# Optimization experiments

Measured on AMD Instinct MI355X. Metric: run time of the kernel, lower is better.

The kernel has to match this reference:

```python
import jax, jax.numpy as jnp
import numpy as np

T_STEPS = 4
TAU = 2.0
EPS = 1e-5
NUM_HEADS = 8
SCALE = 0.125  # hardcoded self.scale in the torch module
SG_ALPHA = 4.0  # spikingjelly default sigmoid surrogate alpha


@jax.custom_vjp
def heaviside(x):
    return (x >= 0.0).astype(x.dtype)

def _hv_fwd(x):
    return heaviside(x), x

def _hv_bwd(x, g):
    s = jax.nn.sigmoid(SG_ALPHA * x)
    return (g * SG_ALPHA * s * (1.0 - s),)

heaviside.defvjp(_hv_fwd, _hv_bwd)


def lif(x_seq, v_th):
    # MultiStepLIFNode: v += (x - v)/tau; spike = H(v - v_th); hard reset to 0 (detached).
    def step(v, x):
        v = v + (x - v) / TAU
        s = heaviside(v - v_th)
        v = v * (1.0 - jax.lax.stop_gradient(s))
        return v, s
    _, out = jax.lax.scan(step, jnp.zeros_like(x_seq[0]), x_seq)
    return out


def bn(x, g, b):
    # BatchNorm1d training-mode stats over (batch, length) per channel; x: (TB, C, N)
    m = jnp.mean(x, axis=(0, 2), keepdims=True)
    var = jnp.mean((x - m) ** 2, axis=(0, 2), keepdims=True)
    return g[None, :, None] * (x - m) * jax.lax.rsqrt(var + EPS) + b[None, :, None]


def _branch(x, w, b, g, beta):
    # linear over channel dim + BN + LIF, then split heads -> (T,B,H,N,d)
    T, B, C, N = x.shape
    y = jnp.einsum('oc,tbcn->tbon', w, x) + b[None, None, :, None]
    y = bn(y.reshape(T * B, C, N), g, beta).reshape(T, B, C, N)
    y = lif(y, 1.0)
    d = C // NUM_HEADS
    return y.transpose(0, 1, 3, 2).reshape(T, B, N, NUM_HEADS, d).transpose(0, 1, 3, 2, 4)


def setup_inputs() -> dict:
    key = jax.random.key(0)
    ks = jax.random.split(key, 6)
    B, C, N = 8, 512, 1024
    bound = float(np.sqrt(6.0 / (3 * C + C)))  # xavier_uniform for (3C, C)
    return {
        'q': jax.random.normal(ks[0], (B, C, N), jnp.float32),
        'k': jax.random.normal(ks[1], (B, C, N), jnp.float32),
        'v': jax.random.normal(ks[2], (B, C, N), jnp.float32),
        'in_proj_w': jax.random.uniform(ks[3], (3 * C, C), jnp.float32, -bound, bound),
        'in_proj_b': jnp.zeros((3 * C,), jnp.float32),
        'q_gamma': jnp.ones((C,), jnp.float32),
        'q_beta': jnp.zeros((C,), jnp.float32),
        'k_gamma': jnp.ones((C,), jnp.float32),
        'k_beta': jnp.zeros((C,), jnp.float32),
        'v_gamma': jnp.ones((C,), jnp.float32),
        'v_beta': jnp.zeros((C,), jnp.float32),
        'proj_w': jax.random.normal(ks[4], (C, C), jnp.float32) * (1.0 / np.sqrt(C)),
        'proj_b': jnp.zeros((C,), jnp.float32),
        'p_gamma': jnp.ones((C,), jnp.float32),
        'p_beta': jnp.zeros((C,), jnp.float32),
    }


def reference(q, k, v, in_proj_w, in_proj_b, q_gamma, q_beta, k_gamma, k_beta,
              v_gamma, v_beta, proj_w, proj_b, p_gamma, p_beta):
    B, C, N = q.shape
    qs = jnp.broadcast_to(q[None], (T_STEPS, B, C, N))
    ks_ = jnp.broadcast_to(k[None], (T_STEPS, B, C, N))
    vs = jnp.broadcast_to(v[None], (T_STEPS, B, C, N))

    qh = _branch(qs, in_proj_w[:C], in_proj_b[:C], q_gamma, q_beta)        # (T,B,H,N,d)
    kh = _branch(ks_, in_proj_w[C:2 * C], in_proj_b[C:2 * C], k_gamma, k_beta)
    vh = _branch(vs, in_proj_w[2 * C:], in_proj_b[2 * C:], v_gamma, v_beta)

    # linear attention: (k^T v) then q @ (k^T v)
    ktv = jnp.einsum('tbhnd,tbhne->tbhde', kh, vh)            # (T,B,H,d,d)
    att = jnp.einsum('tbhnd,tbhde->tbhne', qh, ktv) * SCALE   # (T,B,H,N,d)

    x = att.transpose(0, 1, 2, 4, 3).reshape(T_STEPS, B, C, N)
    x = lif(x, 0.5)  # attn_lif with v_threshold=0.5

    z = jnp.einsum('oc,tbcn->tbon', proj_w, x) + proj_b[None, None, :, None]  # 1x1 conv
    z = bn(z.reshape(T_STEPS * B, C, N), p_gamma, p_beta).reshape(T_STEPS, B, C, N)
    return lif(z, 1.0)
```

## Files before the change

### kernel.cpp

```cpp
#include <hip/hip_runtime.h>

#define C    512
#define NDIM 1024
#define BDIM 8
#define TDIM 4
#define HDIM 8
#define CN   (C*NDIM)
#define BCN  (BDIM*CN)

typedef unsigned short u16;
typedef unsigned int   u32;
typedef unsigned long long u64;
typedef __attribute__((ext_vector_type(8))) short bf8v;
typedef __attribute__((ext_vector_type(4))) float f4v;

__device__ __forceinline__ u16 f2bf(float f) {
    u32 u = __float_as_uint(f);
    u32 r = u + 0x7FFFu + ((u >> 16) & 1u);
    return (u16)(r >> 16);
}
__device__ __forceinline__ float bf2f(u16 h) { return __uint_as_float((u32)h << 16); }

#if defined(__has_builtin)
#if __has_builtin(__builtin_amdgcn_global_load_lds)
#define HAS_GLL 1
#endif
#endif
#ifdef HAS_GLL
#define GLD(gp, lp) __builtin_amdgcn_global_load_lds( \
    (const __attribute__((address_space(1))) u32*)(gp), \
    (__attribute__((address_space(3))) u32*)(lp), 16, 0, 0)
#else
#define GLD(gp, lp) (*(uint4*)(lp) = *(const uint4*)(const void*)(gp))
#endif

__global__ __launch_bounds__(256) void gemm_in3_k(
    const float* __restrict__ W, const float* __restrict__ bias,
    const float* __restrict__ Xq, const float* __restrict__ Xk,
    const float* __restrict__ Xv, float* __restrict__ Y3)
{
    __shared__ float As[16][68];
    __shared__ float Bs[16][136];
    const int tid = threadIdx.x;
    const int bz = blockIdx.z;
    const int br = bz >> 3, b = bz & 7;
    const int m0 = blockIdx.y * 64;
    const int n0 = blockIdx.x * 128;
    const float* Xb = (br == 0 ? Xq : (br == 1 ? Xk : Xv)) + (size_t)b * CN;
    const int rowOff = br * 512;

    const int am = tid >> 2;
    const int ak = (tid & 3) * 4;
    const int bk = tid >> 4;
    const int bn = (tid & 15) * 8;
    const int tx = tid & 15, ty = tid >> 4;

    float acc[4][8];
    #pragma unroll
    for (int i = 0; i < 4; i++)
        #pragma unroll
        for (int j = 0; j < 8; j++) acc[i][j] = 0.f;

    for (int k0 = 0; k0 < 512; k0 += 16) {
        float4 a  = *(const float4*)&W [(size_t)(rowOff + m0 + am) * 512 + k0 + ak];
        float4 b0 = *(const float4*)&Xb[(size_t)(k0 + bk) * NDIM + n0 + bn];
        float4 b1 = *(const float4*)&Xb[(size_t)(k0 + bk) * NDIM + n0 + bn + 4];
        __syncthreads();
        As[ak + 0][am] = a.x; As[ak + 1][am] = a.y;
        As[ak + 2][am] = a.z; As[ak + 3][am] = a.w;
        *(float4*)&Bs[bk][bn]     = b0;
        *(float4*)&Bs[bk][bn + 4] = b1;
        __syncthreads();
        #pragma unroll
        for (int k = 0; k < 16; k++) {
            float av[4], bv[8];
            *(float4*)av = *(const float4*)&As[k][ty * 4];
            *(float4*)&bv[0] = *(const float4*)&Bs[k][tx * 8];
            *(float4*)&bv[4] = *(const float4*)&Bs[k][tx * 8 + 4];
            #pragma unroll
            for (int i = 0; i < 4; i++)
                #pragma unroll
                for (int j = 0; j < 8; j++)
                    acc[i][j] += av[i] * bv[j];
        }
    }
    #pragma unroll
    for (int i = 0; i < 4; i++) {
        float bsv = bias[rowOff + m0 + ty * 4 + i];
        float* yr = Y3 + (size_t)bz * CN + (size_t)(m0 + ty * 4 + i) * NDIM + n0 + tx * 8;
        float4 o0 = make_float4(acc[i][0] + bsv, acc[i][1] + bsv,
                                acc[i][2] + bsv, acc[i][3] + bsv);
        float4 o1 = make_float4(acc[i][4] + bsv, acc[i][5] + bsv,
                                acc[i][6] + bsv, acc[i][7] + bsv);
        *(float4*)&yr[0] = o0;
        *(float4*)&yr[4] = o1;
    }
}

__global__ __launch_bounds__(256) void split_pw_k(
    const float* __restrict__ PW, u16* __restrict__ Ps)
{
    const int idx = blockIdx.x * 256 + threadIdx.x;
    float x = PW[idx];
    u16 h1 = f2bf(x); float r1 = x - bf2f(h1);
    u16 h2 = f2bf(r1); float r2 = r1 - bf2f(h2);
    u16 h3 = f2bf(r2);
    Ps[idx] = h1; Ps[idx + 262144] = h2; Ps[idx + 2 * 262144] = h3;
}

__global__ __launch_bounds__(256, 2) void gemm_proj_mfma(
    const u16* __restrict__ Ps, const unsigned char* __restrict__ spkT,
    float* __restrict__ Z)
{
    __shared__ __align__(16) u16 Ab[2][12288];
    __shared__ __align__(16) u16 Bb[2][4096];
    const int tid = threadIdx.x;
    const int zb = blockIdx.z, t = zb >> 3, bb = zb & 7;
    const int m0 = blockIdx.y * 128, n0 = blockIdx.x * 128;

    u32 aoff[2][3];
    int lofs[2];
    #pragma unroll
    for (int r = 0; r < 2; r++) {
        const int cid = tid + (r << 8);
        const int mm = cid & 15, kg = (cid >> 4) & 3, mt = cid >> 6;
        lofs[r] = cid * 8;
        #pragma unroll
        for (int s = 0; s < 3; s++)
            aoff[r][s] = (u32)s * 262144u + (u32)(m0 + mt * 16 + mm) * 512u + kg * 8;
    }
    auto stageA = [&](int ki2, int p2) {
        const u32 kk = (u32)ki2 << 5;
        #pragma unroll
        for (int r = 0; r < 2; r++)
            #pragma unroll
            for (int s = 0; s < 3; s++)
                GLD(Ps + aoff[r][s] + kk, &Ab[p2][s * 4096 + lofs[r]]);
    };
    const int nn = tid & 15, ntl = (tid >> 4) & 7, seg = tid >> 7;
    const u32 srcB = ((u32)bb * 1024u + (u32)(n0 + ntl * 16 + nn)) * 512u + seg * 16;
    const int ldsB0 = (ntl * 64 + seg * 32 + nn) * 8;
    auto convB = [&](uint4 braw, int p2) {
        u32 bs[4] = {braw.x, braw.y, braw.z, braw.w};
        u32 w[8];
        #pragma unroll
        for (int qq = 0; qq < 4; qq++) {
            u32 v = bs[qq] >> t;
            w[qq * 2 + 0] = ((v & 1u) ? 0x3F80u : 0u) | ((v & 0x100u) ? 0x3F800000u : 0u);
            w[qq * 2 + 1] = (((v >> 16) & 1u) ? 0x3F80u : 0u) | ((v & 0x1000000u) ? 0x3F800000u : 0u);
        }
        *(uint4*)&Bb[p2][ldsB0]       = make_uint4(w[0], w[1], w[2], w[3]);
        *(uint4*)&Bb[p2][ldsB0 + 128] = make_uint4(w[4], w[5], w[6], w[7]);
    };

    const int lane = tid & 63, wv = tid >> 6;
    const int wm = wv >> 1, wn = wv & 1;
    const int q = lane >> 4, ln = lane & 15;
    int afo[4], bfo[4];
    #pragma unroll
    for (int i = 0; i < 4; i++) {
        afo[i] = ((wm * 4 + i) * 64 + q * 16 + ln) * 8;
        bfo[i] = ((wn * 4 + i) * 64 + q * 16 + ln) * 8;
    }

    f4v acc[4][4];
    #pragma unroll
    for (int i = 0; i < 4; i++)
        #pragma unroll
        for (int j = 0; j < 4; j++) acc[i][j] = (f4v){0.f, 0.f, 0.f, 0.f};

    stageA(0, 0);
    convB(*(const uint4*)&spkT[srcB], 0);
    uint4 braw;
    for (int ki = 0; ki < 16; ki++) {
        const int p = ki & 1;
        __syncthreads();
        if (ki < 15) {
            stageA(ki + 1, p ^ 1);
            braw = *(const uint4*)&spkT[srcB + ((u32)(ki + 1) << 5)];
        }
        bf8v bf[4];
        #pragma unroll
        for (int j = 0; j < 4; j++) bf[j] = *(const bf8v*)&Bb[p][bfo[j]];
        #pragma unroll
        for (int sa = 0; sa < 3; sa++) {
            bf8v af[4];
            #pragma unroll
            for (int i = 0; i < 4; i++) af[i] = *(const bf8v*)&Ab[p][sa * 4096 + afo[i]];
            #pragma unroll
            for (int i = 0; i < 4; i++)
                #pragma unroll
                for (int j = 0; j < 4; j++)
                    acc[i][j] = __builtin_amdgcn_mfma_f32_16x16x32_bf16(af[i], bf[j], acc[i][j], 0, 0, 0);
        }
        if (ki < 15) convB(braw, p ^ 1);
    }
    float* Zb = Z + (size_t)zb * CN;
    #pragma unroll
    for (int i = 0; i < 4; i++) {
        const int row = m0 + (wm * 4 + i) * 16 + q * 4;
        #pragma unroll
        for (int g = 0; g < 4; g++) {
            float* zr = Zb + (size_t)(row + g) * 1024 + n0 + ln;
            #pragma unroll
            for (int j = 0; j < 4; j++)
                zr[(wn * 4 + j) * 16] = acc[i][j][g];
        }
    }
}

__global__ __launch_bounds__(256) void chan_sum3_k(
    const float* __restrict__ X3, float* __restrict__ mean3, int outer)
{
    __shared__ float red[256];
    const int gb = blockIdx.x;
    const int o = gb & (C - 1);
    const float* X = X3 + (size_t)(gb >> 9) * BCN;
    const int tid = threadIdx.x;
    const int total = outer * NDIM;
    float s = 0.f;
    for (int i = tid; i < total; i += 256) {
        int ou = i >> 10, n = i & 1023;
        s += X[(size_t)(ou * C + o) * NDIM + n];
    }
    red[tid] = s; __syncthreads();
    for (int off = 128; off > 0; off >>= 1) {
        if (tid < off) red[tid] += red[tid + off];
        __syncthreads();
    }
    if (tid == 0) mean3[gb] = red[0] / (float)total;
}

__global__ __launch_bounds__(256) void chan_var3_k(
    const float* __restrict__ X3, const float* __restrict__ mean3,
    float* __restrict__ rstd3, int outer)
{
    __shared__ float red[256];
    const int gb = blockIdx.x;
    const int o = gb & (C - 1);
    const float* X = X3 + (size_t)(gb >> 9) * BCN;
    const int tid = threadIdx.x;
    const int total = outer * NDIM;
    const float m = mean3[gb];
    float s = 0.f;
    for (int i = tid; i < total; i += 256) {
        int ou = i >> 10, n = i & 1023;
        float d = X[(size_t)(ou * C + o) * NDIM + n] - m;
        s += d * d;
    }
    red[tid] = s; __syncthreads();
    for (int off = 128; off > 0; off >>= 1) {
        if (tid < off) red[tid] += red[tid + off];
        __syncthreads();
    }
    if (tid == 0) rstd3[gb] = 1.f / sqrtf(red[0] / (float)total + 1e-5f);
}

__global__ __launch_bounds__(256) void bn_lif_pack_k(
    const float* __restrict__ Y, const float* __restrict__ mean,
    const float* __restrict__ rstd, const float* __restrict__ gamma,
    const float* __restrict__ beta, unsigned char* __restrict__ spk)
{
    const int idx = blockIdx.x * 256 + threadIdx.x;
    const int o = (idx >> 10) & (C - 1);
    float y = Y[idx];
    float x = gamma[o] * (y - mean[o]);
    x = x * rstd[o] + beta[o];
    float v = 0.f; unsigned bits = 0;
    #pragma unroll
    for (int t = 0; t < 4; t++) {
        v += (x - v) * 0.5f;
        if (v - 1.0f >= 0.f) { bits |= (1u << t); v = 0.f; }
    }
    spk[idx] = (unsigned char)bits;
}

__global__ __launch_bounds__(256) void qpack_k(
    const unsigned char* __restrict__ spk, u64* __restrict__ qm)
{
    __shared__ unsigned char tile[64][80];
    const int tid = threadIdx.x;
    const int bh = blockIdx.x; const int h = bh & 7, b = bh >> 3;
    const int n0 = blockIdx.y * 64;
    {
        int dd = tid >> 2, sg = tid & 3;
        *(uint4*)&tile[dd][sg * 16] =
            *(const uint4*)&spk[(size_t)(b * C + h * 64 + dd) * NDIM + n0 + sg * 16];
    }
    __syncthreads();
    const int lane = tid & 63, wv = tid >> 6;
    for (int i = 0; i < 16; i++) {
        int j = wv * 16 + i;
        unsigned s = tile[lane][j];
        #pragma unroll
        for (int t = 0; t < 4; t++) {
            u64 m = __ballot((s >> t) & 1);
            if (lane == t)
                qm[(size_t)((t * BDIM + b) * HDIM + h) * NDIM + n0 + j] = m;
        }
    }
}

__global__ __launch_bounds__(256) void kv_pack_k(
    const unsigned char* __restrict__ spk, u64* __restrict__ bits)
{
    const int tid = threadIdx.x;
    const int gw = blockIdx.x * 4 + (tid >> 6);
    const int lane = tid & 63;
    const int w = gw & 15, c = (gw >> 4) & (C - 1), b = gw >> 13;
    unsigned s = spk[(size_t)(b * C + c) * NDIM + w * 64 + lane];
    #pragma unroll
    for (int t = 0; t < 4; t++) {
        u64 m = __ballot((s >> t) & 1);
        if (lane == t)
            bits[(size_t)((t * BDIM + b) * C + c) * 16 + w] = m;
    }
}

__global__ __launch_bounds__(256) void ktv_k(
    const u64* __restrict__ kb, const u64* __restrict__ vb,
    u16* __restrict__ ktv)
{
    __shared__ u64 ks[64][17];
    __shared__ u64 vs[64][17];
    const int tid = threadIdx.x;
    const int g = blockIdx.x;
    const int h = g & 7, b = (g >> 3) & 7, t = g >> 6;
    const size_t base = ((size_t)(t * BDIM + b) * C + h * 64) * 16;
    {
        int r = tid >> 2, w0 = (tid & 3) * 4;
        #pragma unroll
        for (int j = 0; j < 4; j++) {
            ks[r][w0 + j] = kb[base + r * 16 + w0 + j];
            vs[r][w0 + j] = vb[base + r * 16 + w0 + j];
        }
    }
    __syncthreads();
    const int dd = tid >> 2, e0 = (tid & 3) * 16;
    u64 kr[16];
    #pragma unroll
    for (int w = 0; w < 16; w++) kr[w] = ks[dd][w];
    #pragma unroll
    for (int i = 0; i < 16; i++) {
        int e = e0 + i;
        int s = 0;
        #pragma unroll
        for (int w = 0; w < 16; w++) s += __popcll(kr[w] & vs[e][w]);
        ktv[(size_t)(g * 64 + dd) * 64 + e] = (u16)s;
    }
}

__global__ __launch_bounds__(256) void att_lif_k(
    const u16* __restrict__ ktv, const u64* __restrict__ qm,
    unsigned char* __restrict__ spkT)
{
    __shared__ u16 ks[4][64][64];
    const int tid = threadIdx.x;
    const int bh = blockIdx.x; const int h = bh & 7, b = bh >> 3;
    const int n0 = blockIdx.y * 64;
    #pragma unroll
    for (int t = 0; t < 4; t++) {
        const u32* src = (const u32*)&ktv[(size_t)((t * BDIM + b) * HDIM + h) * 4096];
        u32* dst = (u32*)&ks[t][0][0];
        #pragma unroll
        for (int j = 0; j < 8; j++) dst[tid + 256 * j] = src[tid + 256 * j];
    }
    __syncthreads();
    const int lane = tid & 63, wv = tid >> 6;
    for (int i = 0; i < 16; i++) {
        const int n = n0 + wv * 16 + i;
        float v = 0.f; unsigned bits = 0;
        #pragma unroll
        for (int t = 0; t < 4; t++) {
            u64 m = qm[(size_t)((t * BDIM + b) * HDIM + h) * NDIM + n];
            int acc = 0;
            while (m) {
                int dd = __ffsll(m) - 1;
                m &= m - 1;
                acc += ks[t][dd][lane];
            }
            float x = (float)acc * 0.125f;
            v += (x - v) * 0.5f;
            if (v - 0.5f >= 0.f) { bits |= (1u << t); v = 0.f; }
        }
        spkT[((size_t)b * 1024 + n) * 512 + h * 64 + lane] = (unsigned char)bits;
    }
}

__global__ __launch_bounds__(256) void final_bn_lif_k(
    float* __restrict__ Z, const float* __restrict__ mean,
    const float* __restrict__ rstd, const float* __restrict__ gamma,
    const float* __restrict__ beta)
{
    const int idx = blockIdx.x * 256 + threadIdx.x;
    const int o = (idx >> 10) & (C - 1);
    const float m = mean[o], rs = rstd[o], g = gamma[o], bt = beta[o];
    float v = 0.f;
    float outs[4];
    #pragma unroll
    for (int t = 0; t < 4; t++) {
        float z = Z[(size_t)t * BCN + idx];
        float x = g * (z - m);
        x = x * rs + bt;
        v += (x - v) * 0.5f;
        float s = (v - 1.0f >= 0.f) ? 1.f : 0.f;
        v *= (1.f - s);
        outs[t] = s;
    }
    #pragma unroll
    for (int t = 0; t < 4; t++) Z[(size_t)t * BCN + idx] = outs[t];
}

extern "C" void kernel_launch(void* const* d_in, const int* in_sizes, int n_in,
                              void* d_out, int out_size, void* d_ws, size_t ws_size,
                              hipStream_t stream)
{
    const float* q     = (const float*)d_in[0];
    const float* k     = (const float*)d_in[1];
    const float* v     = (const float*)d_in[2];
    const float* W     = (const float*)d_in[3];
    const float* Wb    = (const float*)d_in[4];
    const float* qg    = (const float*)d_in[5];
    const float* qb    = (const float*)d_in[6];
    const float* kg    = (const float*)d_in[7];
    const float* kbt   = (const float*)d_in[8];
    const float* vg    = (const float*)d_in[9];
    const float* vbt   = (const float*)d_in[10];
    const float* pw    = (const float*)d_in[11];
    const float* pg    = (const float*)d_in[13];
    const float* pbeta = (const float*)d_in[14];

    char* p = (char*)d_ws;
    unsigned char* spk = (unsigned char*)p; p += (size_t)BCN;
    u64* qmv = (u64*)p;                     p += (size_t)TDIM * BDIM * HDIM * NDIM * 8;
    u64* kbits = (u64*)p;                   p += (size_t)TDIM * BDIM * C * 16 * 8;
    u64* vbits = (u64*)p;                   p += (size_t)TDIM * BDIM * C * 16 * 8;
    u16* ktv = (u16*)p;                     p += (size_t)TDIM * BDIM * HDIM * 64 * 64 * 2;
    float* mean3 = (float*)p;               p += 8192;
    float* rstd3 = (float*)p;               p += 8192;

    float* Y3 = (float*)d_out;
    float* outF = (float*)d_out;
    u16* Ps = (u16*)qmv;
    unsigned char* spkT = spk;

    const float* Gs[3] = {qg, kg, vg};
    const float* Bt[3] = {qb, kbt, vbt};

    gemm_in3_k<<<dim3(8, 8, 24), 256, 0, stream>>>(W, Wb, q, k, v, Y3);
    chan_sum3_k<<<3 * C, 256, 0, stream>>>(Y3, mean3, BDIM);
    chan_var3_k<<<3 * C, 256, 0, stream>>>(Y3, mean3, rstd3, BDIM);
    for (int br = 0; br < 3; ++br) {
        bn_lif_pack_k<<<BCN / 256, 256, 0, stream>>>(Y3 + (size_t)br * BCN,
            mean3 + br * C, rstd3 + br * C, Gs[br], Bt[br], spk);
        if (br == 0)
            qpack_k<<<dim3(64, 16), 256, 0, stream>>>(spk, qmv);
        else
            kv_pack_k<<<16384, 256, 0, stream>>>(spk, br == 1 ? kbits : vbits);
    }
    ktv_k<<<256, 256, 0, stream>>>(kbits, vbits, ktv);
    att_lif_k<<<dim3(64, 16), 256, 0, stream>>>(ktv, qmv, spkT);
    split_pw_k<<<1024, 256, 0, stream>>>(pw, Ps);
    gemm_proj_mfma<<<dim3(8, 4, 32), 256, 0, stream>>>(Ps, spkT, outF);
    chan_sum3_k<<<C, 256, 0, stream>>>(outF, mean3, TDIM * BDIM);
    chan_var3_k<<<C, 256, 0, stream>>>(outF, mean3, rstd3, TDIM * BDIM);
    final_bn_lif_k<<<BCN / 256, 256, 0, stream>>>(outF, mean3, rstd3, pg, pbeta);
}
```

Measured before the change: 585.2 us.

## Enlarge input GEMM tile to 128x128 and fuse BN-LIF with K/V bit packing

The fp32 input projection GEMM moves from 64x128 to 128x128 tiles, each thread computing a 2x2 grid of 4x4 sub-blocks, which raises arithmetic intensity and halves the grid. For the K and V branches, BN+LIF now emits the ballot-packed spike bitmasks directly, which drops the intermediate byte spike buffer and the separate kv_pack kernel launch. Larger per-thread accumulators raise register pressure and may lower occupancy.

Result: faster. 553.4 us (-5.4%).

```diff
diff --git a/kernel.cpp b/kernel.cpp
--- a/kernel.cpp
+++ b/kernel.cpp
@@ -39,62 +39,75 @@
     const float* __restrict__ Xq, const float* __restrict__ Xk,
     const float* __restrict__ Xv, float* __restrict__ Y3)
 {
-    __shared__ float As[16][68];
-    __shared__ float Bs[16][136];
+    __shared__ float As[16][132];
+    __shared__ float Bs[16][132];
     const int tid = threadIdx.x;
     const int bz = blockIdx.z;
     const int br = bz >> 3, b = bz & 7;
-    const int m0 = blockIdx.y * 64;
+    const int m0 = blockIdx.y * 128;
     const int n0 = blockIdx.x * 128;
     const float* Xb = (br == 0 ? Xq : (br == 1 ? Xk : Xv)) + (size_t)b * CN;
     const int rowOff = br * 512;
 
-    const int am = tid >> 2;
-    const int ak = (tid & 3) * 4;
-    const int bk = tid >> 4;
-    const int bn = (tid & 15) * 8;
+    const int ra = tid >> 2, ka = (tid & 3) * 4;
+    const int kb = tid >> 5, nb = (tid & 31) * 4;
     const int tx = tid & 15, ty = tid >> 4;
 
-    float acc[4][8];
-    #pragma unroll
-    for (int i = 0; i < 4; i++)
-        #pragma unroll
-        for (int j = 0; j < 8; j++) acc[i][j] = 0.f;
-
-    for (int k0 = 0; k0 < 512; k0 += 16) {
-        float4 a  = *(const float4*)&W [(size_t)(rowOff + m0 + am) * 512 + k0 + ak];
-        float4 b0 = *(const float4*)&Xb[(size_t)(k0 + bk) * NDIM + n0 + bn];
-        float4 b1 = *(const float4*)&Xb[(size_t)(k0 + bk) * NDIM + n0 + bn + 4];
-        __syncthreads();
-        As[ak + 0][am] = a.x; As[ak + 1][am] = a.y;
-        As[ak + 2][am] = a.z; As[ak + 3][am] = a.w;
-        *(float4*)&Bs[bk][bn]     = b0;
-        *(float4*)&Bs[bk][bn + 4] = b1;
-        __syncthreads();
-        #pragma unroll
-        for (int k = 0; k < 16; k++) {
-            float av[4], bv[8];
-            *(float4*)av = *(const float4*)&As[k][ty * 4];
-            *(float4*)&bv[0] = *(const float4*)&Bs[k][tx * 8];
-            *(float4*)&bv[4] = *(const float4*)&Bs[k][tx * 8 + 4];
+    float acc[2][2][4][4];
+    #pragma unroll
+    for (int mq = 0; mq < 2; mq++)
+        #pragma unroll
+        for (int nq = 0; nq < 2; nq++)
             #pragma unroll
             for (int i = 0; i < 4; i++)
                 #pragma unroll
-                for (int j = 0; j < 8; j++)
-                    acc[i][j] += av[i] * bv[j];
-        }
-    }
-    #pragma unroll
-    for (int i = 0; i < 4; i++) {
-        float bsv = bias[rowOff + m0 + ty * 4 + i];
-        float* yr = Y3 + (size_t)bz * CN + (size_t)(m0 + ty * 4 + i) * NDIM + n0 + tx * 8;
-        float4 o0 = make_float4(acc[i][0] + bsv, acc[i][1] + bsv,
-                                acc[i][2] + bsv, acc[i][3] + bsv);
-        float4 o1 = make_float4(acc[i][4] + bsv, acc[i][5] + bsv,
-                                acc[i][6] + bsv, acc[i][7] + bsv);
-        *(float4*)&yr[0] = o0;
-        *(float4*)&yr[4] = o1;
-    }
+                for (int j = 0; j < 4; j++) acc[mq][nq][i][j] = 0.f;
+
+    for (int k0 = 0; k0 < 512; k0 += 16) {
+        float4 a0 = *(const float4*)&W[(size_t)(rowOff + m0 + ra) * 512 + k0 + ka];
+        float4 a1 = *(const float4*)&W[(size_t)(rowOff + m0 + 64 + ra) * 512 + k0 + ka];
+        float4 b0 = *(const float4*)&Xb[(size_t)(k0 + kb) * NDIM + n0 + nb];
+        float4 b1 = *(const float4*)&Xb[(size_t)(k0 + 8 + kb) * NDIM + n0 + nb];
+        __syncthreads();
+        As[ka + 0][ra] = a0.x; As[ka + 1][ra] = a0.y;
+        As[ka + 2][ra] = a0.z; As[ka + 3][ra] = a0.w;
+        As[ka + 0][64 + ra] = a1.x; As[ka + 1][64 + ra] = a1.y;
+        As[ka + 2][64 + ra] = a1.z; As[ka + 3][64 + ra] = a1.w;
+        *(float4*)&Bs[kb][nb]     = b0;
+        *(float4*)&Bs[kb + 8][nb] = b1;
+        __syncthreads();
+        #pragma unroll
+        for (int k = 0; k < 16; k++) {
+            float av[2][4], bv[2][4];
+            *(float4*)av[0] = *(const float4*)&As[k][ty * 4];
+            *(float4*)av[1] = *(const float4*)&As[k][64 + ty * 4];
+            *(float4*)bv[0] = *(const float4*)&Bs[k][tx * 4];
+            *(float4*)bv[1] = *(const float4*)&Bs[k][64 + tx * 4];
+            #pragma unroll
+            for (int mq = 0; mq < 2; mq++)
+                #pragma unroll
+                for (int nq = 0; nq < 2; nq++)
+                    #pragma unroll
+                    for (int i = 0; i < 4; i++)
+                        #pragma unroll
+                        for (int j = 0; j < 4; j++)
+                            acc[mq][nq][i][j] += av[mq][i] * bv[nq][j];
+        }
+    }
+    #pragma unroll
+    for (int mq = 0; mq < 2; mq++)
+        #pragma unroll
+        for (int i = 0; i < 4; i++) {
+            const int mrow = mq * 64 + ty * 4 + i;
+            float bsv = bias[rowOff + m0 + mrow];
+            float* yr = Y3 + (size_t)bz * CN + (size_t)(m0 + mrow) * NDIM + n0;
+            #pragma unroll
+            for (int nq = 0; nq < 2; nq++) {
+                float4 o4 = make_float4(acc[mq][nq][i][0] + bsv, acc[mq][nq][i][1] + bsv,
+                                        acc[mq][nq][i][2] + bsv, acc[mq][nq][i][3] + bsv);
+                *(float4*)&yr[nq * 64 + tx * 4] = o4;
+            }
+        }
 }
 
 __global__ __launch_bounds__(256) void split_pw_k(
@@ -275,6 +288,33 @@
     spk[idx] = (unsigned char)bits;
 }
 
+__global__ __launch_bounds__(256) void bn_lif_kv_k(
+    const float* __restrict__ Y, const float* __restrict__ mean,
+    const float* __restrict__ rstd, const float* __restrict__ gamma,
+    const float* __restrict__ beta, u64* __restrict__ bits)
+{
+    const int idx = blockIdx.x * 256 + threadIdx.x;
+    const int o = (idx >> 10) & (C - 1);
+    const int b = idx >> 19;
+    const int n = idx & 1023;
+    float y = Y[idx];
+    float x = gamma[o] * (y - mean[o]);
+    x = x * rstd[o] + beta[o];
+    float v = 0.f; unsigned sb = 0;
+    #pragma unroll
+    for (int t = 0; t < 4; t++) {
+        v += (x - v) * 0.5f;
+        if (v - 1.0f >= 0.f) { sb |= (1u << t); v = 0.f; }
+    }
+    const int lane = threadIdx.x & 63;
+    #pragma unroll
+    for (int t = 0; t < 4; t++) {
+        u64 m = __ballot((sb >> t) & 1);
+        if (lane == t)
+            bits[((size_t)(t * BDIM + b) * C + o) * 16 + (n >> 6)] = m;
+    }
+}
+
 __global__ __launch_bounds__(256) void qpack_k(
     const unsigned char* __restrict__ spk, u64* __restrict__ qm)
 {
@@ -298,22 +338,6 @@
             if (lane == t)
                 qm[(size_t)((t * BDIM + b) * HDIM + h) * NDIM + n0 + j] = m;
         }
-    }
-}
-
-__global__ __launch_bounds__(256) void kv_pack_k(
-    const unsigned char* __restrict__ spk, u64* __restrict__ bits)
-{
-    const int tid = threadIdx.x;
-    const int gw = blockIdx.x * 4 + (tid >> 6);
-    const int lane = tid & 63;
-    const int w = gw & 15, c = (gw >> 4) & (C - 1), b = gw >> 13;
-    unsigned s = spk[(size_t)(b * C + c) * NDIM + w * 64 + lane];
-    #pragma unroll
-    for (int t = 0; t < 4; t++) {
-        u64 m = __ballot((s >> t) & 1);
-        if (lane == t)
-            bits[(size_t)((t * BDIM + b) * C + c) * 16 + w] = m;
     }
 }
 
@@ -447,16 +471,19 @@
     const float* Gs[3] = {qg, kg, vg};
     const float* Bt[3] = {qb, kbt, vbt};
 
-    gemm_in3_k<<<dim3(8, 8, 24), 256, 0, stream>>>(W, Wb, q, k, v, Y3);
+    gemm_in3_k<<<dim3(8, 4, 24), 256, 0, stream>>>(W, Wb, q, k, v, Y3);
     chan_sum3_k<<<3 * C, 256, 0, stream>>>(Y3, mean3, BDIM);
     chan_var3_k<<<3 * C, 256, 0, stream>>>(Y3, mean3, rstd3, BDIM);
     for (int br = 0; br < 3; ++br) {
-        bn_lif_pack_k<<<BCN / 256, 256, 0, stream>>>(Y3 + (size_t)br * BCN,
-            mean3 + br * C, rstd3 + br * C, Gs[br], Bt[br], spk);
-        if (br == 0)
+        if (br == 0) {
+            bn_lif_pack_k<<<BCN / 256, 256, 0, stream>>>(Y3,
+                mean3, rstd3, Gs[0], Bt[0], spk);
             qpack_k<<<dim3(64, 16), 256, 0, stream>>>(spk, qmv);
-        else
-            kv_pack_k<<<16384, 256, 0, stream>>>(spk, br == 1 ? kbits : vbits);
+        } else {
+            bn_lif_kv_k<<<BCN / 256, 256, 0, stream>>>(Y3 + (size_t)br * BCN,
+                mean3 + br * C, rstd3 + br * C, Gs[br], Bt[br],
+                br == 1 ? kbits : vbits);
+        }
     }
     ktv_k<<<256, 256, 0, stream>>>(kbits, vbits, ktv);
     att_lif_k<<<dim3(64, 16), 256, 0, stream>>>(ktv, qmv, spkT);
```
